# Optimization experiments

Hardware: AMD Instinct MI355X
Metric: run time of the kernel (lower is better)

The kernel has to match this reference:

```python
import jax, jax.numpy as jnp
import numpy as np

EMBED_DIM = 1024
NUM_HEADS = 16
HEAD_DIM = EMBED_DIM // NUM_HEADS
SCALE = float(np.sqrt(HEAD_DIM))
B, TQ, TK = 2, 2048, 2048


def setup_inputs() -> dict:
    key = jax.random.key(0)
    ks = jax.random.split(key, 16)
    s = 1.0 / np.sqrt(EMBED_DIM)
    inp = {
        "query": jax.random.normal(ks[0], (B, TQ, EMBED_DIM), jnp.float32),
        "key": jax.random.normal(ks[1], (B, TK, EMBED_DIM), jnp.float32),
        "value": jax.random.normal(ks[2], (B, TK, EMBED_DIM), jnp.float32),
        "key_padding_mask": jnp.zeros((B, TK), dtype=bool),
        "Wq": jax.random.uniform(ks[3], (EMBED_DIM, EMBED_DIM), jnp.float32, -s, s),
        "bq": jax.random.uniform(ks[4], (EMBED_DIM,), jnp.float32, -s, s),
        "Wk": jax.random.uniform(ks[5], (EMBED_DIM, EMBED_DIM), jnp.float32, -s, s),
        "bk": jax.random.uniform(ks[6], (EMBED_DIM,), jnp.float32, -s, s),
        "Wv": jax.random.uniform(ks[7], (EMBED_DIM, EMBED_DIM), jnp.float32, -s, s),
        "bv": jax.random.uniform(ks[8], (EMBED_DIM,), jnp.float32, -s, s),
        "Wo": jax.random.uniform(ks[9], (EMBED_DIM, EMBED_DIM), jnp.float32, -s, s),
        "bo": jax.random.uniform(ks[10], (EMBED_DIM,), jnp.float32, -s, s),
        "clr_bias_q": jax.random.normal(ks[11], (NUM_HEADS, 1, HEAD_DIM), jnp.float32) * 0.02,
        "clr_bias_k": jax.random.normal(ks[12], (NUM_HEADS, 1, HEAD_DIM), jnp.float32) * 0.02,
    }
    return inp


def reference(query, key, value, key_padding_mask, Wq, bq, Wk, bk, Wv, bv, Wo, bo,
              clr_bias_q, clr_bias_k):
    Bsz, Tq, _ = query.shape
    Tk = key.shape[1]

    def split_heads(x, W, b, T):
        # Linear (torch convention: x @ W.T + b) then [B, H, T, Dh]
        y = jnp.einsum('bte,fe->btf', x, W) + b
        return y.reshape(Bsz, T, NUM_HEADS, HEAD_DIM).transpose(0, 2, 1, 3)

    q = split_heads(query, Wq, bq, Tq)   # [B,H,Tq,Dh]
    k = split_heads(key, Wk, bk, Tk)     # [B,H,Tk,Dh]
    v = split_heads(value, Wv, bv, Tk)   # [B,H,Tk,Dh]

    # CLR centering + learned bias (Aitchison similarity)
    q_c = q - jnp.mean(q, axis=-1, keepdims=True) + clr_bias_q[None]
    k_c = k - jnp.mean(k, axis=-1, keepdims=True) + clr_bias_k[None]
    scores = jnp.einsum('bhqd,bhkd->bhqk', q_c, k_c) / SCALE  # [B,H,Tq,Tk]

    mask = key_padding_mask[:, None, None, :]  # [B,1,1,Tk], True = ignore
    scores = jnp.where(mask, -jnp.inf, scores)

    attn = jax.nn.softmax(scores, axis=-1)
    out = jnp.einsum('bhqk,bhkd->bhqd', attn, v)
    out = out.transpose(0, 2, 1, 3).reshape(Bsz, Tq, EMBED_DIM)
    return jnp.einsum('bte,fe->btf', out, Wo) + bo
```

## Files before the change

kernel.cpp:

```cpp
#include <hip/hip_runtime.h>
#include <stdint.h>

static constexpr int EMB   = 1024;
static constexpr int HEADS = 16;
static constexpr int HD    = 64;
static constexpr int BATCH = 2;
static constexpr int SEQ   = 2048;
static constexpr int BT    = BATCH * SEQ;
static constexpr float QSC = 0.18033688011112042f;

typedef short   short8  __attribute__((ext_vector_type(8)));
typedef float   float4v __attribute__((ext_vector_type(4)));

__device__ __forceinline__ ushort f2bf(float f) {
    union { float f; uint32_t i; } v; v.f = f;
    uint32_t x = v.i;
    return (ushort)((x + 0x7FFFu + ((x >> 16) & 1u)) >> 16);
}
__device__ __forceinline__ ushort f2bf_rn(float f) {
    union { float f; uint32_t i; } v; v.f = f;
    return (ushort)((v.i + 0x8000u) >> 16);
}
__device__ __forceinline__ uint32_t pack2bf(float lo, float hi) {
    union { float f; uint32_t u; } a, b; a.f = lo; b.f = hi;
    uint32_t ra = a.u + 0x7FFFu + ((a.u >> 16) & 1u);
    uint32_t rb = b.u + 0x7FFFu + ((b.u >> 16) & 1u);
    return (rb & 0xFFFF0000u) | (ra >> 16);
}
__device__ __forceinline__ float fast_exp2(float x) {
#if __has_builtin(__builtin_amdgcn_exp2f)
    return __builtin_amdgcn_exp2f(x);
#else
    return exp2f(x);
#endif
}

__device__ __forceinline__ void async_ld16(const void* g, void* l) {
    __builtin_amdgcn_global_load_lds(
        (const __attribute__((address_space(1))) void*)g,
        (__attribute__((address_space(3))) void*)l,
        16, 0, 0);
}

__global__ void cvt_all(const float* __restrict__ q, const float* __restrict__ k,
                        const float* __restrict__ v,
                        const float* __restrict__ wq, const float* __restrict__ wk,
                        const float* __restrict__ wv, const float* __restrict__ wo,
                        ushort* __restrict__ qb, ushort* __restrict__ kb,
                        ushort* __restrict__ vb,
                        ushort* __restrict__ wqb, ushort* __restrict__ wkb,
                        ushort* __restrict__ wvb, ushort* __restrict__ wob)
{
    int bid = blockIdx.x;
    const float* src; ushort* dst; size_t off;
    if (bid < 6144) {
        int seg = bid >> 11;
        src = seg == 0 ? q : (seg == 1 ? k : v);
        dst = seg == 0 ? qb : (seg == 1 ? kb : vb);
        off = (size_t)(bid & 2047) * 2048;
    } else {
        int t = bid - 6144, seg = t >> 9;
        src = seg == 0 ? wq : (seg == 1 ? wk : (seg == 2 ? wv : wo));
        dst = seg == 0 ? wqb : (seg == 1 ? wkb : (seg == 2 ? wvb : wob));
        off = (size_t)(t & 511) * 2048;
    }
    size_t base = off + (size_t)threadIdx.x * 8;
    float4 a0 = *(const float4*)(src + base);
    float4 a1 = *(const float4*)(src + base + 4);
    uint32_t o[4] = { pack2bf(a0.x, a0.y), pack2bf(a0.z, a0.w),
                      pack2bf(a1.x, a1.y), pack2bf(a1.z, a1.w) };
    *(uint4*)(dst + base) = *(uint4*)o;
}

__device__ __forceinline__ void gemm_core_128(
    const ushort* __restrict__ A, const ushort* __restrict__ W,
    int m0, int n0, int K,
    ushort* As, ushort* Ws,
    int wid, int lane, float4v acc[4][4])
{
    const int lrow8 = lane >> 3;
    const int gc    = (lane & 7) ^ lrow8;
    const ushort* Ab = A + (size_t)m0 * K + gc * 8;
    const ushort* Wb = W + (size_t)n0 * K + gc * 8;
    const int wm = (wid >> 1) * 64;
    const int wn = (wid & 1) * 64;

    for (int k0 = 0; k0 < K; k0 += 64) {
        __syncthreads();
#pragma unroll
        for (int it = 0; it < 4; ++it) {
            int rg = it * 4 + wid;
            int row = rg * 8 + lrow8;
            async_ld16(Ab + (size_t)row * K + k0, &As[rg * 512]);
            async_ld16(Wb + (size_t)row * K + k0, &Ws[rg * 512]);
        }
        __syncthreads();
#pragma unroll
        for (int ks = 0; ks < 2; ++ks) {
            const int c = ks * 4 + (lane >> 4);
            short8 af[4], wf[4];
#pragma unroll
            for (int i = 0; i < 4; i++) {
                int row = wm + i * 16 + (lane & 15);
                af[i] = *(const short8*)&As[row * 64 + ((c ^ (row & 7)) * 8)];
            }
#pragma unroll
            for (int j = 0; j < 4; j++) {
                int row = wn + j * 16 + (lane & 15);
                wf[j] = *(const short8*)&Ws[row * 64 + ((c ^ (row & 7)) * 8)];
            }
#pragma unroll
            for (int i = 0; i < 4; i++)
#pragma unroll
                for (int j = 0; j < 4; j++)
                    acc[i][j] = __builtin_amdgcn_mfma_f32_16x16x32_bf16(af[i], wf[j], acc[i][j], 0, 0, 0);
        }
    }
}

__global__ __launch_bounds__(256, 3)
void gemm_qkv(const ushort* __restrict__ qb, const ushort* __restrict__ kb,
              const ushort* __restrict__ vb,
              const ushort* __restrict__ wqb, const ushort* __restrict__ wkb,
              const ushort* __restrict__ wvb,
              const float* __restrict__ bq, const float* __restrict__ bk,
              const float* __restrict__ bv,
              const float* __restrict__ cbq, const float* __restrict__ cbk,
              ushort* __restrict__ qc, ushort* __restrict__ kc,
              ushort* __restrict__ vt)
{
    __shared__ __align__(16) ushort As[128 * 64];
    __shared__ __align__(16) ushort Ws[128 * 64];

    const int z = blockIdx.z;
    const ushort* A    = z == 0 ? qb  : (z == 1 ? kb  : vb);
    const ushort* W    = z == 0 ? wqb : (z == 1 ? wkb : wvb);
    const float*  bias = z == 0 ? bq  : (z == 1 ? bk  : bv);
    const float*  clrb = z == 0 ? cbq : cbk;
    const float   scale = z == 0 ? QSC : 1.0f;

    const int tid  = threadIdx.x;
    const int wid  = tid >> 6;
    const int lane = tid & 63;
    const int m0 = blockIdx.y * 128;
    const int n0 = blockIdx.x * 128;
    const int wm = (wid >> 1) * 64;
    const int wn = (wid & 1) * 64;

    float4v acc[4][4];
#pragma unroll
    for (int i = 0; i < 4; i++)
#pragma unroll
        for (int j = 0; j < 4; j++) acc[i][j] = (float4v)0.0f;

    gemm_core_128(A, W, m0, n0, EMB, As, Ws, wid, lane, acc);

    const int h = (n0 + wn) >> 6;
#pragma unroll
    for (int i = 0; i < 4; i++) {
        float ys[4][4];
#pragma unroll
        for (int j = 0; j < 4; j++) {
            float bj = bias[n0 + wn + j * 16 + (lane & 15)];
#pragma unroll
            for (int r = 0; r < 4; r++) ys[j][r] = acc[i][j][r] + bj;
        }
        const int rowb = m0 + wm + i * 16 + ((lane >> 4) << 2);

        if (z < 2) {
            float rs[4];
#pragma unroll
            for (int r = 0; r < 4; r++)
                rs[r] = ys[0][r] + ys[1][r] + ys[2][r] + ys[3][r];
#pragma unroll
            for (int r = 0; r < 4; r++)
#pragma unroll
                for (int off = 1; off < 16; off <<= 1)
                    rs[r] += __shfl_xor(rs[r], off, 64);
            ushort* Yb = z == 0 ? qc : kc;
#pragma unroll
            for (int j = 0; j < 4; j++) {
                int d = j * 16 + (lane & 15);
                float cb = clrb[h * HD + d];
#pragma unroll
                for (int r = 0; r < 4; r++) {
                    int row = rowb + r;
                    int b = row >> 11, t = row & (SEQ - 1);
                    Yb[((size_t)(b * HEADS + h) * SEQ + t) * HD + d] =
                        f2bf((ys[j][r] - rs[r] * (1.0f / 64.0f) + cb) * scale);
                }
            }
        } else {
#pragma unroll
            for (int j = 0; j < 4; j++) {
                int d = j * 16 + (lane & 15);
#pragma unroll
                for (int r = 0; r < 4; r++) {
                    int row = rowb + r;
                    int b = row >> 11, t = row & (SEQ - 1);
                    vt[((size_t)(b * HEADS + h) * HD + d) * SEQ + t] = f2bf(ys[j][r]);
                }
            }
        }
    }
}

__global__ __launch_bounds__(256, 3)
void gemm_out(const ushort* __restrict__ A, const ushort* __restrict__ W,
              const float* __restrict__ bias, float* __restrict__ Y)
{
    __shared__ __align__(16) ushort As[128 * 64];
    __shared__ __align__(16) ushort Ws[128 * 64];

    const int tid  = threadIdx.x;
    const int wid  = tid >> 6;
    const int lane = tid & 63;
    const int m0 = blockIdx.y * 128;
    const int n0 = blockIdx.x * 128;
    const int wm = (wid >> 1) * 64;
    const int wn = (wid & 1) * 64;

    float4v acc[4][4];
#pragma unroll
    for (int i = 0; i < 4; i++)
#pragma unroll
        for (int j = 0; j < 4; j++) acc[i][j] = (float4v)0.0f;

    gemm_core_128(A, W, m0, n0, EMB, As, Ws, wid, lane, acc);

#pragma unroll
    for (int i = 0; i < 4; i++) {
        const int rowb = m0 + wm + i * 16 + ((lane >> 4) << 2);
#pragma unroll
        for (int j = 0; j < 4; j++) {
            int col = n0 + wn + j * 16 + (lane & 15);
            float bj = bias[col];
#pragma unroll
            for (int r = 0; r < 4; r++)
                Y[(size_t)(rowb + r) * EMB + col] = acc[i][j][r] + bj;
        }
    }
}

__global__ __launch_bounds__(256, 3)
void attn_kernel(const ushort* __restrict__ qc,
                 const ushort* __restrict__ kc,
                 const ushort* __restrict__ vt,
                 const unsigned char* __restrict__ mask,
                 ushort* __restrict__ out)
{
    __shared__ __align__(16) ushort Ks[2][64 * 64];
    __shared__ __align__(16) ushort Vs[2][64 * 64];
    __shared__ __align__(16) ushort Ps[4][16 * 72];

    const int tid  = threadIdx.x;
    const int wid  = tid >> 6;
    const int lane = tid & 63;

    const int bid = blockIdx.x;
    const int qt = bid & 31;
    const int h  = (bid >> 5) & 15;
    const int b  = bid >> 9;

    const ushort* qbase = qc + ((size_t)(b * HEADS + h)) * SEQ * HD;
    const ushort* kbase = kc + ((size_t)(b * HEADS + h)) * SEQ * HD;
    const ushort* vbase = vt + ((size_t)(b * HEADS + h)) * HD * SEQ;

    const int qrow = qt * 64 + wid * 16 + (lane & 15);
    short8 qf[2];
#pragma unroll
    for (int ks = 0; ks < 2; ++ks)
        qf[ks] = *(const short8*)(qbase + (size_t)qrow * HD + ks * 32 + (lane >> 4) * 8);

    float l_r[4] = {0.f, 0.f, 0.f, 0.f};
    float4v o[4];
#pragma unroll
    for (int j = 0; j < 4; j++) o[j] = (float4v)0.f;

    const int lrow8 = lane >> 3;
    const int gc    = (lane & 7) ^ lrow8;
    ushort* Pw = &Ps[wid][0];

#define STAGE(t, sel)                                                          \
    {                                                                          \
        _Pragma("unroll")                                                      \
        for (int it = 0; it < 2; ++it) {                                       \
            int g   = it * 4 + wid;                                            \
            int row = g * 8 + lrow8;                                           \
            async_ld16(kbase + (size_t)((t) * 64 + row) * HD + gc * 8,         \
                       &Ks[sel][g * 512]);                                     \
            async_ld16(vbase + (size_t)row * SEQ + (t) * 64 + gc * 8,          \
                       &Vs[sel][g * 512]);                                     \
        }                                                                      \
    }

    STAGE(0, 0);
    asm volatile("s_waitcnt vmcnt(0)" ::: "memory");
    __syncthreads();

    int cur = 0;
    for (int kt = 0; kt < SEQ / 64; ++kt) {
        if (kt + 1 < SEQ / 64) STAGE(kt + 1, cur ^ 1);

        const ushort* Kc = &Ks[cur][0];
        const ushort* Vc = &Vs[cur][0];

        float mzv[4];
#pragma unroll
        for (int j = 0; j < 4; ++j)
            mzv[j] = mask[b * SEQ + kt * 64 + j * 16 + (lane & 15)] ? -1e30f : 0.0f;

        float4v s[4];
        __builtin_amdgcn_s_setprio(1);
#pragma unroll
        for (int j = 0; j < 4; j++) {
            s[j] = (float4v)0.f;
#pragma unroll
            for (int ks = 0; ks < 2; ks++) {
                int row = j * 16 + (lane & 15);
                int c   = ks * 4 + (lane >> 4);
                short8 kf = *(const short8*)&Kc[row * 64 + ((c ^ (row & 7)) * 8)];
                s[j] = __builtin_amdgcn_mfma_f32_16x16x32_bf16(qf[ks], kf, s[j], 0, 0, 0);
            }
        }
        __builtin_amdgcn_s_setprio(0);

#pragma unroll
        for (int j = 0; j < 4; j++) {
            int prow = ((lane >> 4) << 2) * 72 + j * 16 + (lane & 15);
#pragma unroll
            for (int r = 0; r < 4; r++) {
                float p = fast_exp2(s[j][r] + mzv[j]);
                l_r[r] += p;
                Pw[prow + r * 72] = f2bf_rn(p);
            }
        }
        asm volatile("s_waitcnt lgkmcnt(0)" ::: "memory");

        short8 pf[2];
#pragma unroll
        for (int ks = 0; ks < 2; ks++)
            pf[ks] = *(const short8*)&Pw[(lane & 15) * 72 + ks * 32 + (lane >> 4) * 8];

        __builtin_amdgcn_s_setprio(1);
#pragma unroll
        for (int j = 0; j < 4; j++) {
            int d = j * 16 + (lane & 15);
#pragma unroll
            for (int ks = 0; ks < 2; ks++) {
                int c = ks * 4 + (lane >> 4);
                short8 vf = *(const short8*)&Vc[d * 64 + ((c ^ (d & 7)) * 8)];
                o[j] = __builtin_amdgcn_mfma_f32_16x16x32_bf16(pf[ks], vf, o[j], 0, 0, 0);
            }
        }
        __builtin_amdgcn_s_setprio(0);

        asm volatile("s_waitcnt vmcnt(0)" ::: "memory");
        __syncthreads();
        cur ^= 1;
    }
#undef STAGE

#pragma unroll
    for (int r = 0; r < 4; r++)
#pragma unroll
        for (int off = 1; off < 16; off <<= 1)
            l_r[r] += __shfl_xor(l_r[r], off, 64);

    const int qrow_out = qt * 64 + wid * 16 + ((lane >> 4) << 2);
#pragma unroll
    for (int j = 0; j < 4; j++) {
        int d = j * 16 + (lane & 15);
#pragma unroll
        for (int r = 0; r < 4; r++) {
            float val = o[j][r] / l_r[r];
            out[((size_t)(b * SEQ + qrow_out + r)) * EMB + h * HD + d] = f2bf(val);
        }
    }
}

extern "C" void kernel_launch(void* const* d_in, const int* in_sizes, int n_in,
                              void* d_out, int out_size, void* d_ws, size_t ws_size,
                              hipStream_t stream)
{
    const float* query = (const float*)d_in[0];
    const float* key_  = (const float*)d_in[1];
    const float* value = (const float*)d_in[2];
    const unsigned char* mask = (const unsigned char*)d_in[3];
    const float* Wq  = (const float*)d_in[4];
    const float* bq  = (const float*)d_in[5];
    const float* Wk  = (const float*)d_in[6];
    const float* bk  = (const float*)d_in[7];
    const float* Wv  = (const float*)d_in[8];
    const float* bv  = (const float*)d_in[9];
    const float* Wo  = (const float*)d_in[10];
    const float* bo  = (const float*)d_in[11];
    const float* cbq = (const float*)d_in[12];
    const float* cbk = (const float*)d_in[13];

    ushort* ws = (ushort*)d_ws;
    const size_t n1 = (size_t)BT * EMB;
    const size_t nw = (size_t)EMB * EMB;
    ushort* qb  = ws;
    ushort* kb  = qb  + n1;
    ushort* vb  = kb  + n1;
    ushort* wqb = vb  + n1;
    ushort* wkb = wqb + nw;
    ushort* wvb = wkb + nw;
    ushort* wob = wvb + nw;
    ushort* qc  = wob + nw;
    ushort* kc  = qc  + n1;
    ushort* vt  = kc  + n1;
    ushort* ao  = qb;

    cvt_all<<<8192, 256, 0, stream>>>(query, key_, value, Wq, Wk, Wv, Wo,
                                      qb, kb, vb, wqb, wkb, wvb, wob);

    dim3 gq(EMB / 128, BT / 128, 3);
    gemm_qkv<<<gq, 256, 0, stream>>>(qb, kb, vb, wqb, wkb, wvb,
                                     bq, bk, bv, cbq, cbk, qc, kc, vt);

    attn_kernel<<<BATCH * HEADS * (SEQ / 64), 256, 0, stream>>>(qc, kc, vt, mask, ao);

    dim3 go(EMB / 128, BT / 128);
    gemm_out<<<go, 256, 0, stream>>>(ao, wob, bo, (float*)d_out);
}
```

Measured before the change: 262.6 us.

## Process two 64-row query tiles per attention block to reuse K/V tiles

```diff
diff --git a/kernel.cpp b/kernel.cpp
--- a/kernel.cpp
+++ b/kernel.cpp
@@ -252,30 +252,47 @@
     __shared__ __align__(16) ushort Ks[2][64 * 64];
     __shared__ __align__(16) ushort Vs[2][64 * 64];
     __shared__ __align__(16) ushort Ps[4][16 * 72];
+    __shared__ __align__(16) float  Msk[SEQ];
 
     const int tid  = threadIdx.x;
     const int wid  = tid >> 6;
     const int lane = tid & 63;
 
     const int bid = blockIdx.x;
-    const int qt = bid & 31;
-    const int h  = (bid >> 5) & 15;
-    const int b  = bid >> 9;
+    const int qt = bid & 15;
+    const int h  = (bid >> 4) & 15;
+    const int b  = bid >> 8;
 
     const ushort* qbase = qc + ((size_t)(b * HEADS + h)) * SEQ * HD;
     const ushort* kbase = kc + ((size_t)(b * HEADS + h)) * SEQ * HD;
     const ushort* vbase = vt + ((size_t)(b * HEADS + h)) * HD * SEQ;
 
-    const int qrow = qt * 64 + wid * 16 + (lane & 15);
-    short8 qf[2];
-#pragma unroll
-    for (int ks = 0; ks < 2; ++ks)
-        qf[ks] = *(const short8*)(qbase + (size_t)qrow * HD + ks * 32 + (lane >> 4) * 8);
-
-    float l_r[4] = {0.f, 0.f, 0.f, 0.f};
-    float4v o[4];
-#pragma unroll
-    for (int j = 0; j < 4; j++) o[j] = (float4v)0.f;
+    {
+        const int k0 = tid * 8;
+        uint2 mv = *(const uint2*)(mask + b * SEQ + k0);
+#pragma unroll
+        for (int i = 0; i < 4; ++i)
+            Msk[k0 + i] = ((mv.x >> (8 * i)) & 0xffu) ? -1e30f : 0.0f;
+#pragma unroll
+        for (int i = 0; i < 4; ++i)
+            Msk[k0 + 4 + i] = ((mv.y >> (8 * i)) & 0xffu) ? -1e30f : 0.0f;
+    }
+
+    short8 qf[2][2];
+#pragma unroll
+    for (int half = 0; half < 2; ++half) {
+        const int qrow = qt * 128 + half * 64 + wid * 16 + (lane & 15);
+#pragma unroll
+        for (int ks = 0; ks < 2; ++ks)
+            qf[half][ks] = *(const short8*)(qbase + (size_t)qrow * HD + ks * 32 + (lane >> 4) * 8);
+    }
+
+    float l_r[2][4];
+    float4v o[2][4];
+#pragma unroll
+    for (int half = 0; half < 2; ++half)
+#pragma unroll
+        for (int j = 0; j < 4; j++) { o[half][j] = (float4v)0.f; l_r[half][j] = 0.f; }
 
     const int lrow8 = lane >> 3;
     const int gc    = (lane & 7) ^ lrow8;
@@ -308,52 +325,55 @@
         float mzv[4];
 #pragma unroll
         for (int j = 0; j < 4; ++j)
-            mzv[j] = mask[b * SEQ + kt * 64 + j * 16 + (lane & 15)] ? -1e30f : 0.0f;
-
-        float4v s[4];
-        __builtin_amdgcn_s_setprio(1);
-#pragma unroll
-        for (int j = 0; j < 4; j++) {
-            s[j] = (float4v)0.f;
-#pragma unroll
-            for (int ks = 0; ks < 2; ks++) {
-                int row = j * 16 + (lane & 15);
-                int c   = ks * 4 + (lane >> 4);
-                short8 kf = *(const short8*)&Kc[row * 64 + ((c ^ (row & 7)) * 8)];
-                s[j] = __builtin_amdgcn_mfma_f32_16x16x32_bf16(qf[ks], kf, s[j], 0, 0, 0);
-            }
-        }
-        __builtin_amdgcn_s_setprio(0);
-
-#pragma unroll
-        for (int j = 0; j < 4; j++) {
-            int prow = ((lane >> 4) << 2) * 72 + j * 16 + (lane & 15);
-#pragma unroll
-            for (int r = 0; r < 4; r++) {
-                float p = fast_exp2(s[j][r] + mzv[j]);
-                l_r[r] += p;
-                Pw[prow + r * 72] = f2bf_rn(p);
-            }
-        }
-        asm volatile("s_waitcnt lgkmcnt(0)" ::: "memory");
-
-        short8 pf[2];
-#pragma unroll
-        for (int ks = 0; ks < 2; ks++)
-            pf[ks] = *(const short8*)&Pw[(lane & 15) * 72 + ks * 32 + (lane >> 4) * 8];
-
-        __builtin_amdgcn_s_setprio(1);
-#pragma unroll
-        for (int j = 0; j < 4; j++) {
-            int d = j * 16 + (lane & 15);
-#pragma unroll
-            for (int ks = 0; ks < 2; ks++) {
-                int c = ks * 4 + (lane >> 4);
-                short8 vf = *(const short8*)&Vc[d * 64 + ((c ^ (d & 7)) * 8)];
-                o[j] = __builtin_amdgcn_mfma_f32_16x16x32_bf16(pf[ks], vf, o[j], 0, 0, 0);
-            }
-        }
-        __builtin_amdgcn_s_setprio(0);
+            mzv[j] = Msk[kt * 64 + j * 16 + (lane & 15)];
+
+#pragma unroll
+        for (int half = 0; half < 2; ++half) {
+            float4v s[4];
+            __builtin_amdgcn_s_setprio(1);
+#pragma unroll
+            for (int j = 0; j < 4; j++) {
+                s[j] = (float4v)0.f;
+#pragma unroll
+                for (int ks = 0; ks < 2; ks++) {
+                    int row = j * 16 + (lane & 15);
+                    int c   = ks * 4 + (lane >> 4);
+                    short8 kf = *(const short8*)&Kc[row * 64 + ((c ^ (row & 7)) * 8)];
+                    s[j] = __builtin_amdgcn_mfma_f32_16x16x32_bf16(qf[half][ks], kf, s[j], 0, 0, 0);
+                }
+            }
+            __builtin_amdgcn_s_setprio(0);
+
+#pragma unroll
+            for (int j = 0; j < 4; j++) {
+                int prow = ((lane >> 4) << 2) * 72 + j * 16 + (lane & 15);
+#pragma unroll
+                for (int r = 0; r < 4; r++) {
+                    float p = fast_exp2(s[j][r] + mzv[j]);
+                    l_r[half][r] += p;
+                    Pw[prow + r * 72] = f2bf_rn(p);
+                }
+            }
+            asm volatile("s_waitcnt lgkmcnt(0)" ::: "memory");
+
+            short8 pf[2];
+#pragma unroll
+            for (int ks = 0; ks < 2; ks++)
+                pf[ks] = *(const short8*)&Pw[(lane & 15) * 72 + ks * 32 + (lane >> 4) * 8];
+
+            __builtin_amdgcn_s_setprio(1);
+#pragma unroll
+            for (int j = 0; j < 4; j++) {
+                int d = j * 16 + (lane & 15);
+#pragma unroll
+                for (int ks = 0; ks < 2; ks++) {
+                    int c = ks * 4 + (lane >> 4);
+                    short8 vf = *(const short8*)&Vc[d * 64 + ((c ^ (d & 7)) * 8)];
+                    o[half][j] = __builtin_amdgcn_mfma_f32_16x16x32_bf16(pf[ks], vf, o[half][j], 0, 0, 0);
+                }
+            }
+            __builtin_amdgcn_s_setprio(0);
+        }
 
         asm volatile("s_waitcnt vmcnt(0)" ::: "memory");
         __syncthreads();
@@ -362,19 +382,22 @@
 #undef STAGE
 
 #pragma unroll
-    for (int r = 0; r < 4; r++)
-#pragma unroll
-        for (int off = 1; off < 16; off <<= 1)
-            l_r[r] += __shfl_xor(l_r[r], off, 64);
-
-    const int qrow_out = qt * 64 + wid * 16 + ((lane >> 4) << 2);
-#pragma unroll
-    for (int j = 0; j < 4; j++) {
-        int d = j * 16 + (lane & 15);
-#pragma unroll
-        for (int r = 0; r < 4; r++) {
-            float val = o[j][r] / l_r[r];
-            out[((size_t)(b * SEQ + qrow_out + r)) * EMB + h * HD + d] = f2bf(val);
+    for (int half = 0; half < 2; ++half) {
+#pragma unroll
+        for (int r = 0; r < 4; r++)
+#pragma unroll
+            for (int off = 1; off < 16; off <<= 1)
+                l_r[half][r] += __shfl_xor(l_r[half][r], off, 64);
+
+        const int qrow_out = qt * 128 + half * 64 + wid * 16 + ((lane >> 4) << 2);
+#pragma unroll
+        for (int j = 0; j < 4; j++) {
+            int d = j * 16 + (lane & 15);
+#pragma unroll
+            for (int r = 0; r < 4; r++) {
+                float val = o[half][j][r] / l_r[half][r];
+                out[((size_t)(b * SEQ + qrow_out + r)) * EMB + h * HD + d] = f2bf(val);
+            }
         }
     }
 }
@@ -420,7 +443,7 @@
     gemm_qkv<<<gq, 256, 0, stream>>>(qb, kb, vb, wqb, wkb, wvb,
                                      bq, bk, bv, cbq, cbk, qc, kc, vt);
 
-    attn_kernel<<<BATCH * HEADS * (SEQ / 64), 256, 0, stream>>>(qc, kc, vt, mask, ao);
+    attn_kernel<<<BATCH * HEADS * (SEQ / 128), 256, 0, stream>>>(qc, kc, vt, mask, ao);
 
     dim3 go(EMB / 128, BT / 128);
     gemm_out<<<go, 256, 0, stream>>>(ao, wob, bo, (float*)d_out);
```

Result: faster. 247.1 us (-5.9%).
